# Kernel tuning notes

Hardware: AMD Instinct MI355X
Metric: run time of the kernel (lower is better)

Reference implementation:

```python
import jax, jax.numpy as jnp
import numpy as np

SIZE = 512
LANG_NUM = 8
B, S, D = 32, 2048, SIZE


def setup_inputs() -> dict:
    key = jax.random.key(0)
    ks = jax.random.split(key, 10)
    sc = 1.0 / np.sqrt(D)
    inp = {
        "old_x": jax.random.normal(ks[0], (B, S, D), jnp.float32),
        "x": jax.random.normal(ks[1], (B, S, D), jnp.float32),
        "lang": jax.random.randint(ks[2], (B,), 0, LANG_NUM, jnp.int32),
        # shared linear (no bias): y = x @ W.T
        "share_W": jax.random.uniform(ks[3], (D, D), jnp.float32, -sc, sc),
        # per-language expert linears (no bias)
        "langs_W": jax.random.uniform(ks[4], (LANG_NUM, D, D), jnp.float32, -sc, sc),
        # per-language gate: layer1 (D->D with bias), layer2 (D->1 with bias)
        "gate_W1": jax.random.uniform(ks[5], (LANG_NUM, D, D), jnp.float32, -sc, sc),
        "gate_b1": jax.random.uniform(ks[6], (LANG_NUM, D), jnp.float32, -sc, sc),
        "gate_W2": jax.random.uniform(ks[7], (LANG_NUM, D), jnp.float32, -sc, sc),
        "gate_b2": jax.random.uniform(ks[8], (LANG_NUM,), jnp.float32, -sc, sc),
    }
    return inp


def reference(old_x, x, lang, share_W, langs_W, gate_W1, gate_b1, gate_W2, gate_b2):
    # shared path: [B,S,D] @ [D,D].T
    share_h = jnp.einsum("bsd,ed->bse", x, share_W)
    # gather per-sample expert weights by lang index
    Wl = langs_W[lang]            # [B,D,D]
    W1 = gate_W1[lang]            # [B,D,D]
    b1 = gate_b1[lang]            # [B,D]
    W2 = gate_W2[lang]            # [B,D]
    b2 = gate_b2[lang]            # [B]
    langs_h = jnp.einsum("bsd,bed->bse", x, Wl)
    # GateLayer on old_x: relu(L1(x)) + x -> L2 -> sigmoid
    h = jax.nn.relu(jnp.einsum("bsd,bed->bse", old_x, W1) + b1[:, None, :]) + old_x
    gate_logit = jnp.einsum("bsd,bd->bs", h, W2) + b2[:, None]
    gate_prob = jax.nn.sigmoid(gate_logit)[:, :, None]   # [B,S,1]
    return share_h * (1.0 - gate_prob) + langs_h * gate_prob
```

## Files before the change

kernel.cpp:

```cpp
#include <hip/hip_runtime.h>
#include <hip/hip_bf16.h>

#define B_ 32
#define S_ 2048
#define D_ 512

typedef __attribute__((ext_vector_type(8))) short bf16x8;
typedef __attribute__((ext_vector_type(4))) float f32x4;
typedef unsigned short ushort_t;

__device__ __forceinline__ float b2f(ushort_t u) {
  union { unsigned int i; float f; } v; v.i = ((unsigned int)u) << 16; return v.f;
}
__device__ __forceinline__ ushort_t f2b(float f) {
  union { float f; unsigned int i; } v; v.f = f;
  return (ushort_t)((v.i + 0x7FFFu + ((v.i >> 16) & 1u)) >> 16);
}

__device__ __forceinline__ f32x4 mfma16(bf16x8 a, bf16x8 b, f32x4 c) {
  return __builtin_amdgcn_mfma_f32_16x16x32_bf16(a, b, c, 0, 0, 0);
}

__global__ void detect_kernel(const unsigned int* __restrict__ w, int* __restrict__ flag) {
  __shared__ int cnt;
  if (threadIdx.x == 0) cnt = 0;
  __syncthreads();
  int c = 0;
  #pragma unroll
  for (int i = 0; i < 4; ++i) {
    unsigned int v = w[threadIdx.x + i * 256];
    unsigned int e = (v >> 7) & 0xFFu;
    if (e >= 110u && e <= 140u) ++c;
  }
  atomicAdd(&cnt, c);
  __syncthreads();
  if (threadIdx.x == 0) flag[0] = (cnt > 512) ? 1 : 0;
}

template <int DT>
__device__ __forceinline__ float ldf(const void* p, size_t idx) {
  if constexpr (DT == 0) return ((const float*)p)[idx];
  else                   return b2f(((const ushort_t*)p)[idx]);
}

template <int DT>
__device__ __forceinline__ void stage_tile(const void* gv, size_t elem_off,
                                           ushort_t* tile, int tid) {
  const int row = tid >> 1, half = tid & 1;
  const size_t base = elem_off + (size_t)row * D_ + half * 16;
  bf16x8 ch0, ch1;
  if constexpr (DT == 0) {
    const float4* src = (const float4*)((const float*)gv + base);
    float4 a = src[0], b = src[1], c = src[2], d = src[3];
    ushort_t t[16];
    t[0] = f2b(a.x); t[1] = f2b(a.y); t[2]  = f2b(a.z); t[3]  = f2b(a.w);
    t[4] = f2b(b.x); t[5] = f2b(b.y); t[6]  = f2b(b.z); t[7]  = f2b(b.w);
    t[8] = f2b(c.x); t[9] = f2b(c.y); t[10] = f2b(c.z); t[11] = f2b(c.w);
    t[12] = f2b(d.x); t[13] = f2b(d.y); t[14] = f2b(d.z); t[15] = f2b(d.w);
    ch0 = *(const bf16x8*)t; ch1 = *(const bf16x8*)(t + 8);
  } else {
    const bf16x8* src = (const bf16x8*)((const ushort_t*)gv + base);
    ch0 = src[0]; ch1 = src[1];
  }
  const int swz = (row >> 1) & 3;
  const int c0 = half * 2, c1 = c0 + 1;
  *(bf16x8*)(tile + row * 32 + ((c0 ^ swz) << 3)) = ch0;
  *(bf16x8*)(tile + row * 32 + ((c1 ^ swz) << 3)) = ch1;
}

__device__ __forceinline__ bf16x8 read_frag(const ushort_t* tile, int row, int quad) {
  int g = quad ^ ((row >> 1) & 3);
  return *(const bf16x8*)(tile + row * 32 + g * 8);
}

template <int DT>
__global__ __launch_bounds__(256, 2)
void gate_kernel(const void* __restrict__ old_x, const int* __restrict__ lang,
                 const void* __restrict__ W1, const void* __restrict__ b1,
                 const void* __restrict__ W2, const void* __restrict__ b2,
                 const int* __restrict__ flag, float* __restrict__ gate) {
  if (flag[0] != DT) return;
  const int b    = blockIdx.y;
  const int s0   = blockIdx.x * 128;
  const int tid  = threadIdx.x;
  const int wave = tid >> 6, lane = tid & 63, quad = lane >> 4, ln = lane & 15;
  const int m_off = (wave >> 1) * 64, n_off = (wave & 1) * 64;
  const int lg = lang[b];

  __shared__ __align__(16) ushort_t As[128 * 32];
  __shared__ __align__(16) ushort_t Bs[128 * 32];
  __shared__ float b1s[512], w2s[512], logit[128];

  for (int i = tid; i < 512; i += 256) {
    b1s[i] = ldf<DT>(b1, (size_t)lg * 512 + i);
    w2s[i] = ldf<DT>(W2, (size_t)lg * 512 + i);
  }
  if (tid < 128) logit[tid] = 0.f;
  __syncthreads();

  {
    const int row = tid >> 1, half = tid & 1;
    const size_t off = ((size_t)b * S_ + s0 + row) * D_ + half * 256;
    float ex = 0.f;
    if constexpr (DT == 0) {
      const float4* xr = (const float4*)((const float*)old_x + off);
      #pragma unroll 8
      for (int c = 0; c < 64; ++c) {
        float4 v = xr[c];
        const float* wp = &w2s[half * 256 + c * 4];
        ex += v.x * wp[0] + v.y * wp[1] + v.z * wp[2] + v.w * wp[3];
      }
    } else {
      const ushort_t* xr = (const ushort_t*)old_x + off;
      #pragma unroll 4
      for (int c = 0; c < 32; ++c) {
        bf16x8 v = *(const bf16x8*)(xr + c * 8);
        #pragma unroll
        for (int j = 0; j < 8; ++j)
          ex += b2f((ushort_t)v[j]) * w2s[half * 256 + c * 8 + j];
      }
    }
    atomicAdd(&logit[row], ex);
  }

  const size_t Aoff = ((size_t)b * S_ + s0) * D_;
  float logacc[16];
  #pragma unroll
  for (int i = 0; i < 16; ++i) logacc[i] = 0.f;

  for (int et = 0; et < 4; ++et) {
    const int e0 = et * 128;
    const size_t Boff = ((size_t)lg * D_ + e0) * D_;
    f32x4 acc[16];
    #pragma unroll
    for (int i = 0; i < 16; ++i) { f32x4 z = {0.f, 0.f, 0.f, 0.f}; acc[i] = z; }

    for (int k0 = 0; k0 < D_; k0 += 32) {
      __syncthreads();
      stage_tile<DT>(old_x, Aoff + k0, As, tid);
      stage_tile<DT>(W1,   Boff + k0, Bs, tid);
      __syncthreads();
      bf16x8 af[4], bfr[4];
      #pragma unroll
      for (int mf = 0; mf < 4; ++mf) af[mf]  = read_frag(As, m_off + mf * 16 + ln, quad);
      #pragma unroll
      for (int nf = 0; nf < 4; ++nf) bfr[nf] = read_frag(Bs, n_off + nf * 16 + ln, quad);
      #pragma unroll
      for (int mf = 0; mf < 4; ++mf)
        #pragma unroll
        for (int nf = 0; nf < 4; ++nf)
          acc[mf * 4 + nf] = mfma16(af[mf], bfr[nf], acc[mf * 4 + nf]);
    }
    #pragma unroll
    for (int nf = 0; nf < 4; ++nf) {
      int e = e0 + n_off + nf * 16 + ln;
      float b1v = b1s[e], w2v = w2s[e];
      #pragma unroll
      for (int mf = 0; mf < 4; ++mf)
        #pragma unroll
        for (int r = 0; r < 4; ++r) {
          float v = acc[mf * 4 + nf][r] + b1v;
          logacc[mf * 4 + r] += fmaxf(v, 0.f) * w2v;
        }
    }
  }

  #pragma unroll
  for (int off = 1; off < 16; off <<= 1)
    #pragma unroll
    for (int i = 0; i < 16; ++i)
      logacc[i] += __shfl_xor(logacc[i], off, 64);
  if (ln == 0) {
    #pragma unroll
    for (int mf = 0; mf < 4; ++mf)
      #pragma unroll
      for (int r = 0; r < 4; ++r)
        atomicAdd(&logit[m_off + mf * 16 + quad * 4 + r], logacc[mf * 4 + r]);
  }
  __syncthreads();
  if (tid < 128) {
    float b2v = ldf<DT>(b2, lg);
    float l = logit[tid] + b2v;
    gate[(size_t)b * S_ + s0 + tid] = 1.f / (1.f + expf(-l));
  }
}

template <int DT>
__global__ __launch_bounds__(256, 2)
void out_kernel(const void* __restrict__ x, const int* __restrict__ lang,
                const void* __restrict__ shareW, const void* __restrict__ langsW,
                const float* __restrict__ gate, const int* __restrict__ flag,
                void* __restrict__ out) {
  if (flag[0] != DT) return;
  const int b    = blockIdx.z;
  const int s0   = blockIdx.y * 128;
  const int e0   = blockIdx.x * 128;
  const int tid  = threadIdx.x;
  const int wave = tid >> 6, lane = tid & 63, quad = lane >> 4, ln = lane & 15;
  const int m_off = (wave >> 1) * 64, n_off = (wave & 1) * 64;
  const int lg = lang[b];

  __shared__ __align__(16) ushort_t As[128 * 32];
  __shared__ __align__(16) ushort_t Ss[128 * 32];
  __shared__ __align__(16) ushort_t Ls[128 * 32];

  const size_t Aoff = ((size_t)b * S_ + s0) * D_;
  const size_t Soff = (size_t)e0 * D_;
  const size_t Loff = ((size_t)lg * D_ + e0) * D_;

  f32x4 accS[16], accL[16];
  #pragma unroll
  for (int i = 0; i < 16; ++i) {
    f32x4 z = {0.f, 0.f, 0.f, 0.f};
    accS[i] = z; accL[i] = z;
  }

  for (int k0 = 0; k0 < D_; k0 += 32) {
    __syncthreads();
    stage_tile<DT>(x,      Aoff + k0, As, tid);
    stage_tile<DT>(shareW, Soff + k0, Ss, tid);
    stage_tile<DT>(langsW, Loff + k0, Ls, tid);
    __syncthreads();
    bf16x8 af[4], sf[4], lf[4];
    #pragma unroll
    for (int mf = 0; mf < 4; ++mf) af[mf] = read_frag(As, m_off + mf * 16 + ln, quad);
    #pragma unroll
    for (int nf = 0; nf < 4; ++nf) {
      sf[nf] = read_frag(Ss, n_off + nf * 16 + ln, quad);
      lf[nf] = read_frag(Ls, n_off + nf * 16 + ln, quad);
    }
    #pragma unroll
    for (int mf = 0; mf < 4; ++mf)
      #pragma unroll
      for (int nf = 0; nf < 4; ++nf) {
        accS[mf * 4 + nf] = mfma16(af[mf], sf[nf], accS[mf * 4 + nf]);
        accL[mf * 4 + nf] = mfma16(af[mf], lf[nf], accL[mf * 4 + nf]);
      }
  }

  #pragma unroll
  for (int mf = 0; mf < 4; ++mf) {
    int srow = s0 + m_off + mf * 16 + quad * 4;
    float gv[4];
    #pragma unroll
    for (int r = 0; r < 4; ++r) gv[r] = gate[(size_t)b * S_ + srow + r];
    #pragma unroll
    for (int nf = 0; nf < 4; ++nf) {
      int col = e0 + n_off + nf * 16 + ln;
      f32x4 cs = accS[mf * 4 + nf], cl = accL[mf * 4 + nf];
      #pragma unroll
      for (int r = 0; r < 4; ++r) {
        float v = cs[r] + gv[r] * (cl[r] - cs[r]);
        size_t idx = ((size_t)b * S_ + srow + r) * D_ + col;
        if constexpr (DT == 0) ((float*)out)[idx] = v;
        else                   ((ushort_t*)out)[idx] = f2b(v);
      }
    }
  }
}

extern "C" void kernel_launch(void* const* d_in, const int* in_sizes, int n_in,
                              void* d_out, int out_size, void* d_ws, size_t ws_size,
                              hipStream_t stream) {
  const void* old_x  = d_in[0];
  const void* x      = d_in[1];
  const int*  lang   = (const int*)d_in[2];
  const void* shareW = d_in[3];
  const void* langsW = d_in[4];
  const void* gW1    = d_in[5];
  const void* gb1    = d_in[6];
  const void* gW2    = d_in[7];
  const void* gb2    = d_in[8];

  float* gate = (float*)d_ws;
  int*   flag = (int*)((char*)d_ws + (size_t)B_ * S_ * sizeof(float));

  detect_kernel<<<1, 256, 0, stream>>>((const unsigned int*)old_x, flag);

  dim3 g1(S_ / 128, B_);
  gate_kernel<0><<<g1, dim3(256), 0, stream>>>(old_x, lang, gW1, gb1, gW2, gb2, flag, gate);
  gate_kernel<1><<<g1, dim3(256), 0, stream>>>(old_x, lang, gW1, gb1, gW2, gb2, flag, gate);

  dim3 g2(D_ / 128, S_ / 128, B_);
  out_kernel<0><<<g2, dim3(256), 0, stream>>>(x, lang, shareW, langsW, gate, flag, d_out);
  out_kernel<1><<<g2, dim3(256), 0, stream>>>(x, lang, shareW, langsW, gate, flag, d_out);
}
```

Measured before the change: 555.0 us.

## Deepen K tile to 64, coalesce staging loads, and swizzle out-kernel block order

The K step doubles to 64, which halves the number of barrier pairs per GEMM. Staging is rewritten so 16 consecutive threads read 16-byte chunks along a row, giving coalesced global loads. fp32 to bf16 conversion now uses a packed hardware convert when the builtin is available. The out kernel moves to a 1D grid that groups 8 sequence tiles per output-column tile, aiming to improve L2 reuse of x and the weights. The cost is double the LDS per block, which may reduce occupancy.

```diff
diff --git a/kernel.cpp b/kernel.cpp
--- a/kernel.cpp
+++ b/kernel.cpp
@@ -15,6 +15,17 @@
 __device__ __forceinline__ ushort_t f2b(float f) {
   union { float f; unsigned int i; } v; v.f = f;
   return (ushort_t)((v.i + 0x7FFFu + ((v.i >> 16) & 1u)) >> 16);
+}
+
+__device__ __forceinline__ unsigned int pk2(float lo, float hi) {
+#if __has_builtin(__builtin_amdgcn_cvt_pk_bf16_f32)
+  typedef __attribute__((ext_vector_type(2))) __bf16 v2bf;
+  union { v2bf v; unsigned int u; } u;
+  u.v = __builtin_amdgcn_cvt_pk_bf16_f32(lo, hi);
+  return u.u;
+#else
+  return (unsigned int)f2b(lo) | ((unsigned int)f2b(hi) << 16);
+#endif
 }
 
 __device__ __forceinline__ f32x4 mfma16(bf16x8 a, bf16x8 b, f32x4 c) {
@@ -44,28 +55,26 @@
 }
 
 template <int DT>
-__device__ __forceinline__ void stage_tile(const void* gv, size_t elem_off,
-                                           ushort_t* tile, int tid) {
-  const int row = tid >> 1, half = tid & 1;
-  const size_t base = elem_off + (size_t)row * D_ + half * 16;
-  bf16x8 ch0, ch1;
-  if constexpr (DT == 0) {
-    const float4* src = (const float4*)((const float*)gv + base);
-    float4 a = src[0], b = src[1], c = src[2], d = src[3];
-    ushort_t t[16];
-    t[0] = f2b(a.x); t[1] = f2b(a.y); t[2]  = f2b(a.z); t[3]  = f2b(a.w);
-    t[4] = f2b(b.x); t[5] = f2b(b.y); t[6]  = f2b(b.z); t[7]  = f2b(b.w);
-    t[8] = f2b(c.x); t[9] = f2b(c.y); t[10] = f2b(c.z); t[11] = f2b(c.w);
-    t[12] = f2b(d.x); t[13] = f2b(d.y); t[14] = f2b(d.z); t[15] = f2b(d.w);
-    ch0 = *(const bf16x8*)t; ch1 = *(const bf16x8*)(t + 8);
-  } else {
-    const bf16x8* src = (const bf16x8*)((const ushort_t*)gv + base);
-    ch0 = src[0]; ch1 = src[1];
-  }
-  const int swz = (row >> 1) & 3;
-  const int c0 = half * 2, c1 = c0 + 1;
-  *(bf16x8*)(tile + row * 32 + ((c0 ^ swz) << 3)) = ch0;
-  *(bf16x8*)(tile + row * 32 + ((c1 ^ swz) << 3)) = ch1;
+__device__ __forceinline__ void stage64(const void* gv, size_t elem_off,
+                                        ushort_t* tile, int tid) {
+  const int kk  = tid & 15;
+  const int sub = kk >> 3;
+  const int c   = (kk >> 1) & 3;
+  const int p   = (kk & 1) * 4;
+  #pragma unroll
+  for (int i = 0; i < 8; ++i) {
+    const int r = (tid >> 4) + i * 16;
+    const size_t g = elem_off + (size_t)r * D_ + kk * 4;
+    uint2 w;
+    if constexpr (DT == 0) {
+      float4 v = *(const float4*)((const float*)gv + g);
+      w.x = pk2(v.x, v.y); w.y = pk2(v.z, v.w);
+    } else {
+      w = *(const uint2*)((const ushort_t*)gv + g);
+    }
+    const int swz = (r >> 1) & 3;
+    *(uint2*)(tile + ((sub * 128 + r) * 32) + ((c ^ swz) << 3) + p) = w;
+  }
 }
 
 __device__ __forceinline__ bf16x8 read_frag(const ushort_t* tile, int row, int quad) {
@@ -87,8 +96,8 @@
   const int m_off = (wave >> 1) * 64, n_off = (wave & 1) * 64;
   const int lg = lang[b];
 
-  __shared__ __align__(16) ushort_t As[128 * 32];
-  __shared__ __align__(16) ushort_t Bs[128 * 32];
+  __shared__ __align__(16) ushort_t As[2 * 128 * 32];
+  __shared__ __align__(16) ushort_t Bs[2 * 128 * 32];
   __shared__ float b1s[512], w2s[512], logit[128];
 
   for (int i = tid; i < 512; i += 256) {
@@ -135,21 +144,26 @@
     #pragma unroll
     for (int i = 0; i < 16; ++i) { f32x4 z = {0.f, 0.f, 0.f, 0.f}; acc[i] = z; }
 
-    for (int k0 = 0; k0 < D_; k0 += 32) {
+    for (int k0 = 0; k0 < D_; k0 += 64) {
       __syncthreads();
-      stage_tile<DT>(old_x, Aoff + k0, As, tid);
-      stage_tile<DT>(W1,   Boff + k0, Bs, tid);
+      stage64<DT>(old_x, Aoff + k0, As, tid);
+      stage64<DT>(W1,   Boff + k0, Bs, tid);
       __syncthreads();
-      bf16x8 af[4], bfr[4];
-      #pragma unroll
-      for (int mf = 0; mf < 4; ++mf) af[mf]  = read_frag(As, m_off + mf * 16 + ln, quad);
-      #pragma unroll
-      for (int nf = 0; nf < 4; ++nf) bfr[nf] = read_frag(Bs, n_off + nf * 16 + ln, quad);
-      #pragma unroll
-      for (int mf = 0; mf < 4; ++mf)
-        #pragma unroll
-        for (int nf = 0; nf < 4; ++nf)
-          acc[mf * 4 + nf] = mfma16(af[mf], bfr[nf], acc[mf * 4 + nf]);
+      #pragma unroll
+      for (int j = 0; j < 2; ++j) {
+        const ushort_t* Aj = As + j * 128 * 32;
+        const ushort_t* Bj = Bs + j * 128 * 32;
+        bf16x8 af[4], bfr[4];
+        #pragma unroll
+        for (int mf = 0; mf < 4; ++mf) af[mf]  = read_frag(Aj, m_off + mf * 16 + ln, quad);
+        #pragma unroll
+        for (int nf = 0; nf < 4; ++nf) bfr[nf] = read_frag(Bj, n_off + nf * 16 + ln, quad);
+        #pragma unroll
+        for (int mf = 0; mf < 4; ++mf)
+          #pragma unroll
+          for (int nf = 0; nf < 4; ++nf)
+            acc[mf * 4 + nf] = mfma16(af[mf], bfr[nf], acc[mf * 4 + nf]);
+      }
     }
     #pragma unroll
     for (int nf = 0; nf < 4; ++nf) {
@@ -179,8 +193,7 @@
   }
   __syncthreads();
   if (tid < 128) {
-    float b2v = ldf<DT>(b2, lg);
-    float l = logit[tid] + b2v;
+    float l = logit[tid] + ldf<DT>(b2, lg);
     gate[(size_t)b * S_ + s0 + tid] = 1.f / (1.f + expf(-l));
   }
 }
@@ -192,17 +205,19 @@
                 const float* __restrict__ gate, const int* __restrict__ flag,
                 void* __restrict__ out) {
   if (flag[0] != DT) return;
-  const int b    = blockIdx.z;
-  const int s0   = blockIdx.y * 128;
-  const int e0   = blockIdx.x * 128;
+  const int id = blockIdx.x;
+  const int e0 = ((id >> 3) & 3) * 128;
+  const int sb = (id >> 5) * 8 + (id & 7);
+  const int b  = sb >> 4;
+  const int s0 = (sb & 15) * 128;
   const int tid  = threadIdx.x;
   const int wave = tid >> 6, lane = tid & 63, quad = lane >> 4, ln = lane & 15;
   const int m_off = (wave >> 1) * 64, n_off = (wave & 1) * 64;
   const int lg = lang[b];
 
-  __shared__ __align__(16) ushort_t As[128 * 32];
-  __shared__ __align__(16) ushort_t Ss[128 * 32];
-  __shared__ __align__(16) ushort_t Ls[128 * 32];
+  __shared__ __align__(16) ushort_t As[2 * 128 * 32];
+  __shared__ __align__(16) ushort_t Ss[2 * 128 * 32];
+  __shared__ __align__(16) ushort_t Ls[2 * 128 * 32];
 
   const size_t Aoff = ((size_t)b * S_ + s0) * D_;
   const size_t Soff = (size_t)e0 * D_;
@@ -215,27 +230,33 @@
     accS[i] = z; accL[i] = z;
   }
 
-  for (int k0 = 0; k0 < D_; k0 += 32) {
+  for (int k0 = 0; k0 < D_; k0 += 64) {
     __syncthreads();
-    stage_tile<DT>(x,      Aoff + k0, As, tid);
-    stage_tile<DT>(shareW, Soff + k0, Ss, tid);
-    stage_tile<DT>(langsW, Loff + k0, Ls, tid);
+    stage64<DT>(x,      Aoff + k0, As, tid);
+    stage64<DT>(shareW, Soff + k0, Ss, tid);
+    stage64<DT>(langsW, Loff + k0, Ls, tid);
     __syncthreads();
-    bf16x8 af[4], sf[4], lf[4];
-    #pragma unroll
-    for (int mf = 0; mf < 4; ++mf) af[mf] = read_frag(As, m_off + mf * 16 + ln, quad);
-    #pragma unroll
-    for (int nf = 0; nf < 4; ++nf) {
-      sf[nf] = read_frag(Ss, n_off + nf * 16 + ln, quad);
-      lf[nf] = read_frag(Ls, n_off + nf * 16 + ln, quad);
-    }
-    #pragma unroll
-    for (int mf = 0; mf < 4; ++mf)
+    #pragma unroll
+    for (int j = 0; j < 2; ++j) {
+      const ushort_t* Aj = As + j * 128 * 32;
+      const ushort_t* Sj = Ss + j * 128 * 32;
+      const ushort_t* Lj = Ls + j * 128 * 32;
+      bf16x8 af[4], sf[4], lf[4];
+      #pragma unroll
+      for (int mf = 0; mf < 4; ++mf) af[mf] = read_frag(Aj, m_off + mf * 16 + ln, quad);
       #pragma unroll
       for (int nf = 0; nf < 4; ++nf) {
-        accS[mf * 4 + nf] = mfma16(af[mf], sf[nf], accS[mf * 4 + nf]);
-        accL[mf * 4 + nf] = mfma16(af[mf], lf[nf], accL[mf * 4 + nf]);
-      }
+        sf[nf] = read_frag(Sj, n_off + nf * 16 + ln, quad);
+        lf[nf] = read_frag(Lj, n_off + nf * 16 + ln, quad);
+      }
+      #pragma unroll
+      for (int mf = 0; mf < 4; ++mf)
+        #pragma unroll
+        for (int nf = 0; nf < 4; ++nf) {
+          accS[mf * 4 + nf] = mfma16(af[mf], sf[nf], accS[mf * 4 + nf]);
+          accL[mf * 4 + nf] = mfma16(af[mf], lf[nf], accL[mf * 4 + nf]);
+        }
+    }
   }
 
   #pragma unroll
@@ -281,7 +302,6 @@
   gate_kernel<0><<<g1, dim3(256), 0, stream>>>(old_x, lang, gW1, gb1, gW2, gb2, flag, gate);
   gate_kernel<1><<<g1, dim3(256), 0, stream>>>(old_x, lang, gW1, gb1, gW2, gb2, flag, gate);
 
-  dim3 g2(D_ / 128, S_ / 128, B_);
-  out_kernel<0><<<g2, dim3(256), 0, stream>>>(x, lang, shareW, langsW, gate, flag, d_out);
-  out_kernel<1><<<g2, dim3(256), 0, stream>>>(x, lang, shareW, langsW, gate, flag, d_out);
-}
+  out_kernel<0><<<dim3(2048), dim3(256), 0, stream>>>(x, lang, shareW, langsW, gate, flag, d_out);
+  out_kernel<1><<<dim3(2048), dim3(256), 0, stream>>>(x, lang, shareW, langsW, gate, flag, d_out);
+}
```

After: 847.3 us. 52.7% more time.
